# Performance work log

Measured on AMD Instinct MI355X. Metric: run time of the kernel, lower is better.

Reference implementation:

```python
import jax, jax.numpy as jnp
import numpy as np


def setup_inputs() -> dict:
    key = jax.random.key(0)
    k1, k2, k3, k4 = jax.random.split(key, 4)
    B, NITER, NSIZE, DIM = 4096, 8, 32, 64
    return {
        "self_vectors": jax.random.normal(k1, (B, NITER, DIM), dtype=jnp.float32),
        "neighbor_vectors": jax.random.normal(k2, (B, NITER * NSIZE, DIM), dtype=jnp.float32),
        "neighbor_relations": jax.random.normal(k3, (B, NITER * NSIZE, DIM), dtype=jnp.float32),
        "user_embeddings": jax.random.normal(k4, (B, DIM), dtype=jnp.float32),
        "neighbor_size": NSIZE,
    }


def reference(self_vectors, neighbor_vectors, neighbor_relations, user_embeddings, neighbor_size):
    B, neighbor_iter, dim = self_vectors.shape
    # reshape flat neighbor axis -> (B, neighbor_iter, neighbor_size, dim)
    nv = neighbor_vectors.reshape(B, neighbor_iter, neighbor_size, dim)
    nr = neighbor_relations.reshape(B, neighbor_iter, neighbor_size, dim)
    ue = user_embeddings.reshape(B, 1, 1, dim)
    # user-relation attention score per neighbor: mean over dim
    scores = jnp.mean(ue * nr, axis=-1)                       # [B, niter, nsize]
    weights = jax.nn.softmax(scores, axis=-1)[..., None]      # [B, niter, nsize, 1]
    # softmax-weighted neighbors, then mean over neighbor axis
    neighbors_aggregated = jnp.mean(weights * nv, axis=2)     # [B, niter, dim]
    return jax.nn.relu(neighbors_aggregated)
```

## Files before the change

### kernel.cpp

```cpp
#include <hip/hip_runtime.h>


constexpr int DIM = 64;
constexpr int NSIZE = 32;

__global__ __launch_bounds__(256) void Aggregator_kernel(
    const float* __restrict__ nv,
    const float* __restrict__ nr,
    const float* __restrict__ ue,
    float* __restrict__ out,
    int niter, int ntasks) {
  int wave = (int)((blockIdx.x * blockDim.x + threadIdx.x) >> 6);
  if (wave >= ntasks) return;
  int lane = (int)(threadIdx.x & 63);
  int b = wave / niter;
  int q = lane & 15;

  const float4* nr4 = (const float4*)(nr + (size_t)wave * (NSIZE * DIM));
  const float4* nv4 = (const float4*)(nv + (size_t)wave * (NSIZE * DIM));

  float4 a[8], v[8];
#pragma unroll
  for (int j = 0; j < 8; ++j) a[j] = nr4[j * 64 + lane];
  float4 u = ((const float4*)(ue + (size_t)b * DIM))[q];
#pragma unroll
  for (int j = 0; j < 8; ++j) v[j] = nv4[j * 64 + lane];

  float sc[8];
#pragma unroll
  for (int j = 0; j < 8; ++j) {
    float p = a[j].x * u.x;
    p = fmaf(a[j].y, u.y, p);
    p = fmaf(a[j].z, u.z, p);
    p = fmaf(a[j].w, u.w, p);
#pragma unroll
    for (int k = 1; k < 16; k <<= 1) p += __shfl_xor(p, k);
    sc[j] = p * (1.0f / DIM);
  }

  float m = sc[0];
#pragma unroll
  for (int j = 1; j < 8; ++j) m = fmaxf(m, sc[j]);
  m = fmaxf(m, __shfl_xor(m, 16));
  m = fmaxf(m, __shfl_xor(m, 32));
  float e[8];
  float z = 0.f;
#pragma unroll
  for (int j = 0; j < 8; ++j) {
    e[j] = __expf(sc[j] - m);
    z += e[j];
  }
  z += __shfl_xor(z, 16);
  z += __shfl_xor(z, 32);
  float inv = 1.0f / (z * (float)NSIZE);

  float4 acc = make_float4(0.f, 0.f, 0.f, 0.f);
#pragma unroll
  for (int j = 0; j < 8; ++j) {
    float w = e[j] * inv;
    acc.x = fmaf(w, v[j].x, acc.x);
    acc.y = fmaf(w, v[j].y, acc.y);
    acc.z = fmaf(w, v[j].z, acc.z);
    acc.w = fmaf(w, v[j].w, acc.w);
  }
#pragma unroll
  for (int k = 16; k < 64; k <<= 1) {
    acc.x += __shfl_xor(acc.x, k);
    acc.y += __shfl_xor(acc.y, k);
    acc.z += __shfl_xor(acc.z, k);
    acc.w += __shfl_xor(acc.w, k);
  }

  if (lane < 16) {
    float4 r = make_float4(fmaxf(acc.x, 0.f), fmaxf(acc.y, 0.f),
                           fmaxf(acc.z, 0.f), fmaxf(acc.w, 0.f));
    ((float4*)(out + (size_t)wave * DIM))[q] = r;
  }
}

extern "C" void kernel_launch(void* const* d_in, const int* in_sizes, int n_in,
                              void* d_out, int out_size, void* d_ws, size_t ws_size,
                              hipStream_t stream) {
  const float* nv = (const float*)d_in[1];
  const float* nr = (const float*)d_in[2];
  const float* ue = (const float*)d_in[3];
  float* out = (float*)d_out;

  int ntasks = in_sizes[0] / DIM;
  int niter  = in_sizes[0] / in_sizes[3];
  int blocks = (ntasks + 3) / 4;
  Aggregator_kernel<<<blocks, 256, 0, stream>>>(nv, nr, ue, out, niter, ntasks);
}
```

Baseline: 514.4 us.

## Process four tasks per wave with double-buffered register prefetch

Each wave now handles four strided tasks and uses two register buffers, so the loads for the next task are issued before the current task is computed. The grid is four times smaller and the launch bounds request two blocks per CU. This aims to hide global-memory latency by keeping more loads in flight per wave. In exchange it doubles register use, which can lower occupancy and reduce memory-level parallelism across waves.

```diff
diff --git a/kernel.cpp b/kernel.cpp
--- a/kernel.cpp
+++ b/kernel.cpp
@@ -3,29 +3,26 @@
 
 constexpr int DIM = 64;
 constexpr int NSIZE = 32;
+constexpr int NT = 4;
+constexpr int WPB = 4;
 
-__global__ __launch_bounds__(256) void Aggregator_kernel(
-    const float* __restrict__ nv,
-    const float* __restrict__ nr,
-    const float* __restrict__ ue,
-    float* __restrict__ out,
-    int niter, int ntasks) {
-  int wave = (int)((blockIdx.x * blockDim.x + threadIdx.x) >> 6);
-  if (wave >= ntasks) return;
-  int lane = (int)(threadIdx.x & 63);
-  int b = wave / niter;
-  int q = lane & 15;
+__device__ __forceinline__ void load_task(
+    const float4* __restrict__ nr4, const float4* __restrict__ nv4,
+    const float* __restrict__ ue, int t, int niter, int lane, int q,
+    float4 (&a)[8], float4 (&v)[8], float4& u) {
+  const float4* A = nr4 + (size_t)t * 512;
+  const float4* V = nv4 + (size_t)t * 512;
+#pragma unroll
+  for (int j = 0; j < 8; ++j) a[j] = A[j * 64 + lane];
+#pragma unroll
+  for (int j = 0; j < 8; ++j) v[j] = V[j * 64 + lane];
+  int b = t / niter;
+  u = ((const float4*)(ue + (size_t)b * DIM))[q];
+}
 
-  const float4* nr4 = (const float4*)(nr + (size_t)wave * (NSIZE * DIM));
-  const float4* nv4 = (const float4*)(nv + (size_t)wave * (NSIZE * DIM));
-
-  float4 a[8], v[8];
-#pragma unroll
-  for (int j = 0; j < 8; ++j) a[j] = nr4[j * 64 + lane];
-  float4 u = ((const float4*)(ue + (size_t)b * DIM))[q];
-#pragma unroll
-  for (int j = 0; j < 8; ++j) v[j] = nv4[j * 64 + lane];
-
+__device__ __forceinline__ void compute_task(
+    const float4 (&a)[8], const float4 (&v)[8], const float4& u,
+    float* __restrict__ out, int t, int lane, int q) {
   float sc[8];
 #pragma unroll
   for (int j = 0; j < 8; ++j) {
@@ -37,7 +34,6 @@
     for (int k = 1; k < 16; k <<= 1) p += __shfl_xor(p, k);
     sc[j] = p * (1.0f / DIM);
   }
-
   float m = sc[0];
 #pragma unroll
   for (int j = 1; j < 8; ++j) m = fmaxf(m, sc[j]);
@@ -70,12 +66,41 @@
     acc.z += __shfl_xor(acc.z, k);
     acc.w += __shfl_xor(acc.w, k);
   }
-
   if (lane < 16) {
     float4 r = make_float4(fmaxf(acc.x, 0.f), fmaxf(acc.y, 0.f),
                            fmaxf(acc.z, 0.f), fmaxf(acc.w, 0.f));
-    ((float4*)(out + (size_t)wave * DIM))[q] = r;
+    ((float4*)(out + (size_t)t * DIM))[q] = r;
   }
+}
+
+__global__ __launch_bounds__(256, 2) void Aggregator_kernel(
+    const float* __restrict__ nv, const float* __restrict__ nr,
+    const float* __restrict__ ue, float* __restrict__ out,
+    int niter, int ntasks) {
+  int wave = (int)(blockIdx.x * WPB + (threadIdx.x >> 6));
+  int nwaves = (int)(gridDim.x * WPB);
+  int lane = (int)(threadIdx.x & 63);
+  int q = lane & 15;
+
+  const float4* nr4 = (const float4*)nr;
+  const float4* nv4 = (const float4*)nv;
+
+  int t0 = wave;
+  int t1 = wave + nwaves;
+  int t2 = wave + 2 * nwaves;
+  int t3 = wave + 3 * nwaves;
+
+  float4 a0[8], v0[8], u0;
+  float4 a1[8], v1[8], u1;
+
+  if (t0 < ntasks) load_task(nr4, nv4, ue, t0, niter, lane, q, a0, v0, u0);
+  if (t1 < ntasks) load_task(nr4, nv4, ue, t1, niter, lane, q, a1, v1, u1);
+  if (t0 < ntasks) compute_task(a0, v0, u0, out, t0, lane, q);
+  if (t2 < ntasks) load_task(nr4, nv4, ue, t2, niter, lane, q, a0, v0, u0);
+  if (t1 < ntasks) compute_task(a1, v1, u1, out, t1, lane, q);
+  if (t3 < ntasks) load_task(nr4, nv4, ue, t3, niter, lane, q, a1, v1, u1);
+  if (t2 < ntasks) compute_task(a0, v0, u0, out, t2, lane, q);
+  if (t3 < ntasks) compute_task(a1, v1, u1, out, t3, lane, q);
 }
 
 extern "C" void kernel_launch(void* const* d_in, const int* in_sizes, int n_in,
@@ -88,6 +113,6 @@
 
   int ntasks = in_sizes[0] / DIM;
   int niter  = in_sizes[0] / in_sizes[3];
-  int blocks = (ntasks + 3) / 4;
+  int blocks = (ntasks + WPB * NT - 1) / (WPB * NT);
   Aggregator_kernel<<<blocks, 256, 0, stream>>>(nv, nr, ue, out, niter, ntasks);
 }
```

After: 519.0 us. Within noise of the previous version (+0.9%).
